# Kernel optimization log

Hardware: AMD Instinct MI355X
Metric: run time of the kernel (lower is better)

## Reference

```python
import jax, jax.numpy as jnp
import numpy as np

COST_KEYPOINT = 1.0
COST_GIOU = 1.0


def box_cxcyczwhd_to_xyzxyz(b):
    c, s = b[..., :3], b[..., 3:]
    return jnp.concatenate([c - 0.5 * s, c + 0.5 * s], axis=-1)


def generalized_3d_box_iou(b1, b2):
    # b1: [N,6], b2: [M,6], both xyzxyz. Returns [N,M] GIoU.
    vol1 = jnp.prod(b1[:, 3:] - b1[:, :3], axis=-1)
    vol2 = jnp.prod(b2[:, 3:] - b2[:, :3], axis=-1)
    lt = jnp.maximum(b1[:, None, :3], b2[None, :, :3])
    rb = jnp.minimum(b1[:, None, 3:], b2[None, :, 3:])
    inter = jnp.prod(jnp.maximum(rb - lt, 0.0), axis=-1)
    union = vol1[:, None] + vol2[None, :] - inter
    iou = inter / union
    elt = jnp.minimum(b1[:, None, :3], b2[None, :, :3])
    erb = jnp.maximum(b1[:, None, 3:], b2[None, :, 3:])
    evol = jnp.prod(jnp.maximum(erb - elt, 0.0), axis=-1)
    return iou - (evol - union) / evol


@jax.jit
def compute_cost(pred_keypoints, pred_boxes, tgt_boxes, tgt_keypoints):
    bs, Q = pred_keypoints.shape[:2]
    out_kp = pred_keypoints.reshape(bs * Q, -1)            # [bs*Q, K*3]
    out_boxes = pred_boxes.reshape(bs * Q, 6)
    tgt_b = tgt_boxes.reshape(-1, 6)                        # [T_total, 6]
    tgt_kp = tgt_keypoints.reshape(tgt_b.shape[0], -1)      # [T_total, K*3]
    xyz_min = box_cxcyczwhd_to_xyzxyz(tgt_b)[:, :3]
    K3 = tgt_kp.shape[-1]
    kp = tgt_kp.reshape(-1, K3 // 3, 3)
    # normalize keypoints relative to box min-corner and box size
    dist_kp = ((kp - xyz_min[:, None, :]) / tgt_b[:, None, 3:]).reshape(-1, K3)
    # L1 cdist: [bs*Q, T_total]
    cost_kp = jnp.sum(jnp.abs(out_kp[:, None, :] - dist_kp[None, :, :]), axis=-1)
    cost_giou = -generalized_3d_box_iou(
        box_cxcyczwhd_to_xyzxyz(out_boxes), box_cxcyczwhd_to_xyzxyz(tgt_b))
    C = COST_KEYPOINT * cost_kp + COST_GIOU * cost_giou
    return C.reshape(bs, Q, -1)


def _lap(cost):
    # Jonker-Volgenant shortest-augmenting-path LAP (scipy-style).
    # cost: [n, m] with n <= m. Returns (arange(n), col4row).
    cost = np.asarray(cost, dtype=np.float64)
    n, m = cost.shape
    u = np.zeros(n)
    v = np.zeros(m)
    col4row = np.full(n, -1, np.int64)
    row4col = np.full(m, -1, np.int64)
    for curRow in range(n):
        path = np.full(m, -1, np.int64)
        SR = np.zeros(n, bool)
        SC = np.zeros(m, bool)
        shortest = np.full(m, np.inf)
        minVal = 0.0
        i = curRow
        sink = -1
        while sink == -1:
            SR[i] = True
            idx = np.where(~SC)[0]
            r = minVal + cost[i, idx] - u[i] - v[idx]
            better = r < shortest[idx]
            shortest[idx[better]] = r[better]
            path[idx[better]] = i
            jloc = np.argmin(shortest[idx])
            j = idx[jloc]
            minVal = shortest[j]
            SC[j] = True
            if row4col[j] == -1:
                sink = j
            else:
                i = row4col[j]
        u[curRow] += minVal
        mask = SR.copy()
        mask[curRow] = False
        u[mask] += minVal - shortest[col4row[mask]]
        v[SC] -= minVal - shortest[SC]
        j = sink
        while True:
            i = path[j]
            row4col[j] = i
            col4row[i], j = j, col4row[i]
            if i == curRow:
                break
    return np.arange(n), col4row


def _linear_sum_assignment(cost):
    # cost: [Q, T] with Q >= T; mirrors scipy's transpose handling:
    # returns (row_ind sorted ascending, matching col_ind).
    rows, cols = _lap(cost.T)  # rows = arange(T) targets, cols = query ids
    order = np.argsort(cols)
    return cols[order], rows[order]


def setup_inputs() -> dict:
    key = jax.random.key(0)
    k1, k2, k3, k4, k5, k6 = jax.random.split(key, 6)
    BS, Q, T, K = 16, 300, 50, 17
    pred_keypoints = jax.random.normal(k1, (BS, Q, K * 3), dtype=jnp.float32)
    pred_boxes = jnp.concatenate([
        jax.random.uniform(k2, (BS, Q, 3), dtype=jnp.float32),
        jax.random.uniform(k3, (BS, Q, 3), dtype=jnp.float32) * 0.5 + 0.05,
    ], axis=-1)
    tgt_boxes = jnp.concatenate([
        jax.random.uniform(k4, (BS, T, 3), dtype=jnp.float32),
        jax.random.uniform(k5, (BS, T, 3), dtype=jnp.float32) * 0.5 + 0.05,
    ], axis=-1)
    tgt_keypoints = jax.random.uniform(k6, (BS, T, K * 3), dtype=jnp.float32)
    return {"pred_keypoints": pred_keypoints, "pred_boxes": pred_boxes,
            "tgt_boxes": tgt_boxes, "tgt_keypoints": tgt_keypoints}


def reference(pred_keypoints, pred_boxes, tgt_boxes, tgt_keypoints):
    C = compute_cost(pred_keypoints, pred_boxes, tgt_boxes, tgt_keypoints)
    Cn = np.asarray(C)
    bs, Q, _ = Cn.shape
    T = tgt_boxes.shape[1]
    # per-image block of the column-split cost matrix, as in torch C.split(sizes, -1)
    idx = []
    for b in range(bs):
        i, j = _linear_sum_assignment(Cn[b, :, b * T:(b + 1) * T])
        idx.append(np.stack([i, j]))
    indices = jnp.asarray(np.stack(idx), dtype=jnp.int32)  # [bs, 2, T]
    return C, indices
```

## Files before the change

### kernel.cpp

```cpp
#include <hip/hip_runtime.h>
#include <math.h>

#define BSZ 16
#define NQ 300
#define NT 50
#define K3 51
#define NPRED (BSZ*NQ)
#define NTGT  (BSZ*NT)
#define NC    (NPRED*NTGT)
#define TSTRIDE 301
#define SMEMF 15232


template<int CTRL, int RMASK>
__device__ __forceinline__ unsigned int dpp_minstep_u32(unsigned int x) {
    unsigned int o = (unsigned int)__builtin_amdgcn_update_dpp((int)x, (int)x, CTRL, RMASK, 0xF, false);
    return (x < o) ? x : o;
}
__device__ __forceinline__ unsigned int wave_min_u32(unsigned int x) {
    x = dpp_minstep_u32<0xB1, 0xF>(x);
    x = dpp_minstep_u32<0x4E, 0xF>(x);
    x = dpp_minstep_u32<0x141, 0xF>(x);
    x = dpp_minstep_u32<0x140, 0xF>(x);
    x = dpp_minstep_u32<0x142, 0xA>(x);
    x = dpp_minstep_u32<0x143, 0xC>(x);
    return (unsigned int)__builtin_amdgcn_readlane((int)x, 63);
}
__device__ __forceinline__ float readlane_f32(float x, int lane) {
    return __int_as_float(__builtin_amdgcn_readlane(__float_as_int(x), lane));
}
__device__ __forceinline__ unsigned int f32key(float x) {
    unsigned int b = (unsigned int)__float_as_int(x);
    return b ^ (((int)b < 0) ? 0xFFFFFFFFu : 0x80000000u);
}

__device__ __forceinline__ float giou_cost(
    float plt0, float plt1, float plt2, float prb0, float prb1, float prb2, float pvol,
    float tlt0, float tlt1, float tlt2, float trb0, float trb1, float trb2, float tvol)
{
    float inter = fmaxf(fminf(prb0,trb0) - fmaxf(plt0,tlt0), 0.f);
    inter *= fmaxf(fminf(prb1,trb1) - fmaxf(plt1,tlt1), 0.f);
    inter *= fmaxf(fminf(prb2,trb2) - fmaxf(plt2,tlt2), 0.f);
    float evol = fmaxf(fmaxf(prb0,trb0) - fminf(plt0,tlt0), 0.f);
    evol *= fmaxf(fmaxf(prb1,trb1) - fminf(plt1,tlt1), 0.f);
    evol *= fmaxf(fmaxf(prb2,trb2) - fminf(plt2,tlt2), 0.f);
    float uni = pvol + tvol - inter;
    return inter/uni - (evol - uni)/evol;
}

__global__ __launch_bounds__(1024) void fused_kernel(
    const float* __restrict__ pred_kp, const float* __restrict__ pred_boxes,
    const float* __restrict__ tgt_boxes, const float* __restrict__ tgt_kp,
    float* __restrict__ C, float* __restrict__ out_idx)
{
    __shared__ __align__(16) float smem[SMEMF];
    const int bid = blockIdx.x;
    const int tid = threadIdx.x;

    if (bid >= BSZ) {
        const int cb = bid - BSZ;
        const int pb = cb % 75, tb = cb / 75;
        const int p0 = pb * 64, t0 = tb * 80;
        float* s_dk   = smem;
        float* s_tbox = smem + 4480;
        float* s_pk   = smem + 5440;

        if (tid < 80) {
            const float* tb6 = tgt_boxes + (size_t)(t0 + tid) * 6;
            float c0=tb6[0], c1=tb6[1], c2=tb6[2], s0=tb6[3], s1=tb6[4], s2=tb6[5];
            float l0=c0-0.5f*s0, l1=c1-0.5f*s1, l2=c2-0.5f*s2;
            float r0=c0+0.5f*s0, r1=c1+0.5f*s1, r2=c2+0.5f*s2;
            float* tw = s_tbox + tid*12;
            tw[0]=l0; tw[1]=l1; tw[2]=l2; tw[3]=r0; tw[4]=r1; tw[5]=r2;
            tw[6]=(r0-l0)*(r1-l1)*(r2-l2);
            tw[9]=s0; tw[10]=s1; tw[11]=s2;
        }
        __syncthreads();
        for (int e = tid; e < 80*K3; e += 1024) {
            int t = e / K3; int c = e - t*K3; int d = c % 3;
            float kp = tgt_kp[(size_t)t0*K3 + e];
            s_dk[t*56 + c] = (kp - s_tbox[t*12 + d]) / s_tbox[t*12 + 9 + d];
        }
        for (int e = tid; e < 64*K3; e += 1024)
            s_pk[e] = pred_kp[(size_t)p0*K3 + e];
        __syncthreads();

        const int pl = tid & 63, g = tid >> 6;
        float a[K3];
        #pragma unroll
        for (int c = 0; c < K3; ++c) a[c] = s_pk[pl*K3 + c];
        const int p = p0 + pl;
        const float* pb6 = pred_boxes + (size_t)p * 6;
        float pc0=pb6[0],pc1=pb6[1],pc2=pb6[2],ps0=pb6[3],ps1=pb6[4],ps2=pb6[5];
        float plt0=pc0-0.5f*ps0, plt1=pc1-0.5f*ps1, plt2=pc2-0.5f*ps2;
        float prb0=pc0+0.5f*ps0, prb1=pc1+0.5f*ps1, prb2=pc2+0.5f*ps2;
        float pvol=(prb0-plt0)*(prb1-plt1)*(prb2-plt2);

        #pragma unroll
        for (int k = 0; k < 5; ++k) {
            int tl = g*5 + k;
            const float* bbp = s_dk + tl*56;
            float sum = 0.f;
            #pragma unroll
            for (int c4 = 0; c4 < 12; ++c4) {
                float4 q = *(const float4*)(bbp + 4*c4);
                sum += fabsf(a[4*c4+0] - q.x);
                sum += fabsf(a[4*c4+1] - q.y);
                sum += fabsf(a[4*c4+2] - q.z);
                sum += fabsf(a[4*c4+3] - q.w);
            }
            sum += fabsf(a[48] - bbp[48]);
            sum += fabsf(a[49] - bbp[49]);
            sum += fabsf(a[50] - bbp[50]);
            const float* tw = s_tbox + tl*12;
            float g_ = giou_cost(plt0,plt1,plt2,prb0,prb1,prb2,pvol,
                                 tw[0],tw[1],tw[2],tw[3],tw[4],tw[5],tw[6]);
            C[(size_t)p*NTGT + (t0+tl)] = sum - g_;
        }
        return;
    }

    const int b = bid;
    const int ln = tid & 63, w = tid >> 6;
    const int bq0 = b*NQ, bt0 = b*NT;
    float* tile = smem;

    for (int e = tid; e < NT*K3; e += 1024)
        tile[e] = tgt_kp[(size_t)bt0*K3 + e];
    __syncthreads();

    float dk[K3];
    float tl0=0,tl1=0,tl2=0,tr0=0,tr1=0,tr2=0,tvol=0;
    if (ln < NT) {
        const float* tb6 = tgt_boxes + (size_t)(bt0+ln)*6;
        float c0=tb6[0],c1=tb6[1],c2=tb6[2],s0=tb6[3],s1=tb6[4],s2=tb6[5];
        tl0=c0-0.5f*s0; tl1=c1-0.5f*s1; tl2=c2-0.5f*s2;
        tr0=c0+0.5f*s0; tr1=c1+0.5f*s1; tr2=c2+0.5f*s2;
        tvol=(tr0-tl0)*(tr1-tl1)*(tr2-tl2);
        #pragma unroll
        for (int c = 0; c < K3; ++c) {
            int d = c % 3;
            float L = (d==0)?tl0:((d==1)?tl1:tl2);
            float S = (d==0)?s0:((d==1)?s1:s2);
            dk[c] = (tile[ln*K3 + c] - L) / S;
        }
    }
    __syncthreads();

    for (int p = w; p < NQ; p += 16) {
        const float* prow = pred_kp + (size_t)(bq0+p)*K3;
        const float* pb6  = pred_boxes + (size_t)(bq0+p)*6;
        float pc0=pb6[0],pc1=pb6[1],pc2=pb6[2],ps0=pb6[3],ps1=pb6[4],ps2=pb6[5];
        float plt0=pc0-0.5f*ps0, plt1=pc1-0.5f*ps1, plt2=pc2-0.5f*ps2;
        float prb0=pc0+0.5f*ps0, prb1=pc1+0.5f*ps1, prb2=pc2+0.5f*ps2;
        float pvol=(prb0-plt0)*(prb1-plt1)*(prb2-plt2);
        if (ln < NT) {
            float sum = 0.f;
            #pragma unroll
            for (int c = 0; c < K3; ++c) sum += fabsf(prow[c] - dk[c]);
            float g_ = giou_cost(plt0,plt1,plt2,prb0,prb1,prb2,pvol,
                                 tl0,tl1,tl2,tr0,tr1,tr2,tvol);
            tile[ln*TSTRIDE + p] = sum - g_;
        }
    }
    __syncthreads();

    float* s_rmv = smem + 15072;
    int*   s_rmc = (int*)(smem + 15136);
    for (int r = w; r < NT; r += 16) {
        float bv = __builtin_inff(); int bj = 0x7fffffff;
        #pragma unroll
        for (int s = 0; s < 5; ++s) {
            int j = ln + 64*s;
            if (j < NQ) {
                float cv = tile[r*TSTRIDE + j];
                if (cv < bv || (cv == bv && j < bj)) { bv = cv; bj = j; }
            }
        }
        #pragma unroll
        for (int off = 32; off > 0; off >>= 1) {
            float ov = __shfl_xor(bv, off);
            int   oj = __shfl_xor(bj, off);
            if (ov < bv || (ov == bv && oj < bj)) { bv = ov; bj = oj; }
        }
        if (ln == 0) { s_rmv[r] = bv; s_rmc[r] = bj; }
    }
    __syncthreads();
    if (w != 0) return;

    float u = 0.0f;
    int c4r = -1;
    if (ln < NT) u = s_rmv[ln];
    int wantj = (ln < NT) ? s_rmc[ln] : -1;
    for (int r = 0; r < NT; ++r) {
        int j = __builtin_amdgcn_readlane(wantj, r);
        unsigned long long taken = __ballot((ln < NT) && (c4r == j));
        if (taken == 0ull && ln == r) c4r = j;
    }

    float v5[5], sh[5];
    int pth[5];
    #pragma unroll
    for (int s = 0; s < 5; ++s) v5[s] = 0.0f;
    const float FINF = __builtin_inff();

    for (int curRow = 0; curRow < NT; ++curRow) {
        if (__builtin_amdgcn_readlane(c4r, curRow) >= 0) continue;
        #pragma unroll
        for (int s = 0; s < 5; ++s) { sh[s] = FINF; pth[s] = -1; }
        int SCm = (ln < 60) ? 0 : 0x1F;
        unsigned long long SRmask = 0ull;
        int i = curRow;
        float minVal = 0.0f;
        int sink = -1;

        while (true) {
            SRmask |= (1ull << i);
            float cf[5] = {0.f, 0.f, 0.f, 0.f, 0.f};
            if (ln < 60) {
                const float* rp = tile + i*TSTRIDE + 5*ln;
                cf[0]=rp[0]; cf[1]=rp[1]; cf[2]=rp[2]; cf[3]=rp[3]; cf[4]=rp[4];
            }
            float u_i = readlane_f32(u, i);
            float e[5];
            #pragma unroll
            for (int s = 0; s < 5; ++s) {
                bool open = ((SCm >> s) & 1) == 0;
                float r = ((minVal + cf[s]) - u_i) - v5[s];
                bool upd = open && (r < sh[s]);
                sh[s]  = upd ? r : sh[s];
                pth[s] = upd ? i : pth[s];
                e[s] = open ? sh[s] : FINF;
            }
            float lmin = fminf(fminf(fminf(e[0], e[1]), fminf(e[2], e[3])), e[4]);
            int aslot = (e[0]==lmin) ? 0 : (e[1]==lmin) ? 1 :
                        (e[2]==lmin) ? 2 : (e[3]==lmin) ? 3 : 4;
            unsigned int kmin = wave_min_u32(f32key(lmin));
            unsigned long long cands = __ballot(f32key(lmin) == kmin);
            int lstar = __builtin_ctzll(cands);
            float m = readlane_f32(lmin, lstar);
            int jstar = 5*lstar + __builtin_amdgcn_readlane(aslot, lstar);
            minVal = m;
            unsigned long long mm = __ballot((ln < NT) && (c4r == jstar));
            if (ln == lstar) SCm |= 1 << (jstar - 5*lstar);
            if (mm == 0ull) { sink = jstar; break; }
            i = __builtin_ctzll(mm);
        }

        int cg  = (c4r >= 0) ? c4r : 0;
        int gow = cg / 5, gsl = cg - 5*gow;
        float g0 = __shfl(sh[0], gow);
        float g1 = __shfl(sh[1], gow);
        float g2 = __shfl(sh[2], gow);
        float g3 = __shfl(sh[3], gow);
        float g4 = __shfl(sh[4], gow);
        float gg = g0;
        gg = (gsl == 1) ? g1 : gg;
        gg = (gsl == 2) ? g2 : gg;
        gg = (gsl == 3) ? g3 : gg;
        gg = (gsl == 4) ? g4 : gg;
        bool inSR = (ln < NT) && ((SRmask >> ln) & 1ull);
        float du = (ln == curRow) ? minVal : (minVal - gg);
        u = inSR ? (u + du) : u;
        #pragma unroll
        for (int s = 0; s < 5; ++s) {
            bool closed = ((SCm >> s) & 1) != 0;
            v5[s] = closed ? (v5[s] - (minVal - sh[s])) : v5[s];
        }

        int j = sink;
        while (true) {
            int ow2 = j / 5, sl2 = j - 5*ow2;
            int ps = pth[0];
            ps = (sl2==1) ? pth[1] : ps;
            ps = (sl2==2) ? pth[2] : ps;
            ps = (sl2==3) ? pth[3] : ps;
            ps = (sl2==4) ? pth[4] : ps;
            int ii = __builtin_amdgcn_readlane(ps, ow2);
            int jj = __builtin_amdgcn_readlane(c4r, ii);
            if (ln == ii) c4r = j;
            j = jj;
            if (ii == curRow) break;
        }
    }

    int* smem_i = (int*)smem;
    __threadfence_block();
    if (ln < NT) smem_i[ln] = c4r;
    __threadfence_block();
    int myc = c4r;
    int rank = 0;
    for (int s2 = 0; s2 < NT; ++s2) rank += (smem_i[s2] < myc) ? 1 : 0;
    if (ln < NT) {
        out_idx[b*(2*NT) + rank]      = (float)myc;
        out_idx[b*(2*NT) + NT + rank] = (float)ln;
    }
}

extern "C" void kernel_launch(void* const* d_in, const int* in_sizes, int n_in,
                              void* d_out, int out_size, void* d_ws, size_t ws_size,
                              hipStream_t stream)
{
    const float* pred_kp    = (const float*)d_in[0];
    const float* pred_boxes = (const float*)d_in[1];
    const float* tgt_boxes  = (const float*)d_in[2];
    const float* tgt_kp     = (const float*)d_in[3];
    float* C   = (float*)d_out;
    float* idx = C + NC;
    fused_kernel<<<dim3(BSZ + 750), 1024, 0, stream>>>(
        pred_kp, pred_boxes, tgt_boxes, tgt_kp, C, idx);
}
```

Before: 127.9 us.

## Split fused kernel into cost and LAP kernels with register-resident cost rows

Splits the single fused launch into a cost-matrix kernel and a separate LAP kernel. The LAP kernel now runs with 256 threads and reads its per-image block back from the global C instead of recomputing it. It also preloads each lane's 5 columns for all 50 rows into registers and picks the row with a switch, instead of reading shared memory on every augmenting step. The goal is to free the cost kernel from the LAP's heavy shared-memory and register footprint and to shorten the serial LAP inner loop, at the cost of an extra launch and a dependency on global memory.

```diff
diff --git a/kernel.cpp b/kernel.cpp
--- a/kernel.cpp
+++ b/kernel.cpp
@@ -9,7 +9,6 @@
 #define NTGT  (BSZ*NT)
 #define NC    (NPRED*NTGT)
 #define TSTRIDE 301
-#define SMEMF 15232
 
 
 template<int CTRL, int RMASK>
@@ -48,126 +47,96 @@
     return inter/uni - (evol - uni)/evol;
 }
 
-__global__ __launch_bounds__(1024) void fused_kernel(
+__global__ __launch_bounds__(1024) void cost_kernel(
     const float* __restrict__ pred_kp, const float* __restrict__ pred_boxes,
     const float* __restrict__ tgt_boxes, const float* __restrict__ tgt_kp,
-    float* __restrict__ C, float* __restrict__ out_idx)
+    float* __restrict__ C)
 {
-    __shared__ __align__(16) float smem[SMEMF];
-    const int bid = blockIdx.x;
+    __shared__ __align__(16) float smem[8704];
+    const int cb = blockIdx.x;
     const int tid = threadIdx.x;
-
-    if (bid >= BSZ) {
-        const int cb = bid - BSZ;
-        const int pb = cb % 75, tb = cb / 75;
-        const int p0 = pb * 64, t0 = tb * 80;
-        float* s_dk   = smem;
-        float* s_tbox = smem + 4480;
-        float* s_pk   = smem + 5440;
-
-        if (tid < 80) {
-            const float* tb6 = tgt_boxes + (size_t)(t0 + tid) * 6;
-            float c0=tb6[0], c1=tb6[1], c2=tb6[2], s0=tb6[3], s1=tb6[4], s2=tb6[5];
-            float l0=c0-0.5f*s0, l1=c1-0.5f*s1, l2=c2-0.5f*s2;
-            float r0=c0+0.5f*s0, r1=c1+0.5f*s1, r2=c2+0.5f*s2;
-            float* tw = s_tbox + tid*12;
-            tw[0]=l0; tw[1]=l1; tw[2]=l2; tw[3]=r0; tw[4]=r1; tw[5]=r2;
-            tw[6]=(r0-l0)*(r1-l1)*(r2-l2);
-            tw[9]=s0; tw[10]=s1; tw[11]=s2;
-        }
-        __syncthreads();
-        for (int e = tid; e < 80*K3; e += 1024) {
-            int t = e / K3; int c = e - t*K3; int d = c % 3;
-            float kp = tgt_kp[(size_t)t0*K3 + e];
-            s_dk[t*56 + c] = (kp - s_tbox[t*12 + d]) / s_tbox[t*12 + 9 + d];
-        }
-        for (int e = tid; e < 64*K3; e += 1024)
-            s_pk[e] = pred_kp[(size_t)p0*K3 + e];
-        __syncthreads();
-
-        const int pl = tid & 63, g = tid >> 6;
-        float a[K3];
-        #pragma unroll
-        for (int c = 0; c < K3; ++c) a[c] = s_pk[pl*K3 + c];
-        const int p = p0 + pl;
-        const float* pb6 = pred_boxes + (size_t)p * 6;
-        float pc0=pb6[0],pc1=pb6[1],pc2=pb6[2],ps0=pb6[3],ps1=pb6[4],ps2=pb6[5];
-        float plt0=pc0-0.5f*ps0, plt1=pc1-0.5f*ps1, plt2=pc2-0.5f*ps2;
-        float prb0=pc0+0.5f*ps0, prb1=pc1+0.5f*ps1, prb2=pc2+0.5f*ps2;
-        float pvol=(prb0-plt0)*(prb1-plt1)*(prb2-plt2);
-
-        #pragma unroll
-        for (int k = 0; k < 5; ++k) {
-            int tl = g*5 + k;
-            const float* bbp = s_dk + tl*56;
-            float sum = 0.f;
-            #pragma unroll
-            for (int c4 = 0; c4 < 12; ++c4) {
-                float4 q = *(const float4*)(bbp + 4*c4);
-                sum += fabsf(a[4*c4+0] - q.x);
-                sum += fabsf(a[4*c4+1] - q.y);
-                sum += fabsf(a[4*c4+2] - q.z);
-                sum += fabsf(a[4*c4+3] - q.w);
-            }
-            sum += fabsf(a[48] - bbp[48]);
-            sum += fabsf(a[49] - bbp[49]);
-            sum += fabsf(a[50] - bbp[50]);
-            const float* tw = s_tbox + tl*12;
-            float g_ = giou_cost(plt0,plt1,plt2,prb0,prb1,prb2,pvol,
-                                 tw[0],tw[1],tw[2],tw[3],tw[4],tw[5],tw[6]);
-            C[(size_t)p*NTGT + (t0+tl)] = sum - g_;
-        }
-        return;
-    }
-
-    const int b = bid;
+    const int pb = cb % 75, tb = cb / 75;
+    const int p0 = pb * 64, t0 = tb * 80;
+    float* s_dk   = smem;
+    float* s_tbox = smem + 4480;
+    float* s_pk   = smem + 5440;
+
+    if (tid < 80) {
+        const float* tb6 = tgt_boxes + (size_t)(t0 + tid) * 6;
+        float c0=tb6[0], c1=tb6[1], c2=tb6[2], s0=tb6[3], s1=tb6[4], s2=tb6[5];
+        float l0=c0-0.5f*s0, l1=c1-0.5f*s1, l2=c2-0.5f*s2;
+        float r0=c0+0.5f*s0, r1=c1+0.5f*s1, r2=c2+0.5f*s2;
+        float* tw = s_tbox + tid*12;
+        tw[0]=l0; tw[1]=l1; tw[2]=l2; tw[3]=r0; tw[4]=r1; tw[5]=r2;
+        tw[6]=(r0-l0)*(r1-l1)*(r2-l2);
+        tw[9]=s0; tw[10]=s1; tw[11]=s2;
+    }
+    __syncthreads();
+    for (int e = tid; e < 80*K3; e += 1024) {
+        int t = e / K3; int c = e - t*K3; int d = c % 3;
+        float kp = tgt_kp[(size_t)t0*K3 + e];
+        s_dk[t*56 + c] = (kp - s_tbox[t*12 + d]) / s_tbox[t*12 + 9 + d];
+    }
+    for (int e = tid; e < 64*K3; e += 1024)
+        s_pk[e] = pred_kp[(size_t)p0*K3 + e];
+    __syncthreads();
+
+    const int pl = tid & 63, g = tid >> 6;
+    float a[K3];
+    #pragma unroll
+    for (int c = 0; c < K3; ++c) a[c] = s_pk[pl*K3 + c];
+    const int p = p0 + pl;
+    const float* pb6 = pred_boxes + (size_t)p * 6;
+    float pc0=pb6[0],pc1=pb6[1],pc2=pb6[2],ps0=pb6[3],ps1=pb6[4],ps2=pb6[5];
+    float plt0=pc0-0.5f*ps0, plt1=pc1-0.5f*ps1, plt2=pc2-0.5f*ps2;
+    float prb0=pc0+0.5f*ps0, prb1=pc1+0.5f*ps1, prb2=pc2+0.5f*ps2;
+    float pvol=(prb0-plt0)*(prb1-plt1)*(prb2-plt2);
+
+    #pragma unroll
+    for (int k = 0; k < 5; ++k) {
+        int tl = g*5 + k;
+        const float* bbp = s_dk + tl*56;
+        float sum = 0.f;
+        #pragma unroll
+        for (int c4 = 0; c4 < 12; ++c4) {
+            float4 q = *(const float4*)(bbp + 4*c4);
+            sum += fabsf(a[4*c4+0] - q.x);
+            sum += fabsf(a[4*c4+1] - q.y);
+            sum += fabsf(a[4*c4+2] - q.z);
+            sum += fabsf(a[4*c4+3] - q.w);
+        }
+        sum += fabsf(a[48] - bbp[48]);
+        sum += fabsf(a[49] - bbp[49]);
+        sum += fabsf(a[50] - bbp[50]);
+        const float* tw = s_tbox + tl*12;
+        float g_ = giou_cost(plt0,plt1,plt2,prb0,prb1,prb2,pvol,
+                             tw[0],tw[1],tw[2],tw[3],tw[4],tw[5],tw[6]);
+        C[(size_t)p*NTGT + (t0+tl)] = sum - g_;
+    }
+}
+
+#define RCASE(I) case I: cf[0]=rt[5*I+0]; cf[1]=rt[5*I+1]; cf[2]=rt[5*I+2]; \
+                          cf[3]=rt[5*I+3]; cf[4]=rt[5*I+4]; break;
+
+__global__ __launch_bounds__(256, 1) void lap_kernel(
+    const float* __restrict__ C, float* __restrict__ out_idx)
+{
+    __shared__ __align__(16) float smem[15232];
+    const int b = blockIdx.x;
+    const int tid = threadIdx.x;
     const int ln = tid & 63, w = tid >> 6;
     const int bq0 = b*NQ, bt0 = b*NT;
     float* tile = smem;
 
-    for (int e = tid; e < NT*K3; e += 1024)
-        tile[e] = tgt_kp[(size_t)bt0*K3 + e];
-    __syncthreads();
-
-    float dk[K3];
-    float tl0=0,tl1=0,tl2=0,tr0=0,tr1=0,tr2=0,tvol=0;
-    if (ln < NT) {
-        const float* tb6 = tgt_boxes + (size_t)(bt0+ln)*6;
-        float c0=tb6[0],c1=tb6[1],c2=tb6[2],s0=tb6[3],s1=tb6[4],s2=tb6[5];
-        tl0=c0-0.5f*s0; tl1=c1-0.5f*s1; tl2=c2-0.5f*s2;
-        tr0=c0+0.5f*s0; tr1=c1+0.5f*s1; tr2=c2+0.5f*s2;
-        tvol=(tr0-tl0)*(tr1-tl1)*(tr2-tl2);
-        #pragma unroll
-        for (int c = 0; c < K3; ++c) {
-            int d = c % 3;
-            float L = (d==0)?tl0:((d==1)?tl1:tl2);
-            float S = (d==0)?s0:((d==1)?s1:s2);
-            dk[c] = (tile[ln*K3 + c] - L) / S;
-        }
-    }
-    __syncthreads();
-
-    for (int p = w; p < NQ; p += 16) {
-        const float* prow = pred_kp + (size_t)(bq0+p)*K3;
-        const float* pb6  = pred_boxes + (size_t)(bq0+p)*6;
-        float pc0=pb6[0],pc1=pb6[1],pc2=pb6[2],ps0=pb6[3],ps1=pb6[4],ps2=pb6[5];
-        float plt0=pc0-0.5f*ps0, plt1=pc1-0.5f*ps1, plt2=pc2-0.5f*ps2;
-        float prb0=pc0+0.5f*ps0, prb1=pc1+0.5f*ps1, prb2=pc2+0.5f*ps2;
-        float pvol=(prb0-plt0)*(prb1-plt1)*(prb2-plt2);
-        if (ln < NT) {
-            float sum = 0.f;
-            #pragma unroll
-            for (int c = 0; c < K3; ++c) sum += fabsf(prow[c] - dk[c]);
-            float g_ = giou_cost(plt0,plt1,plt2,prb0,prb1,prb2,pvol,
-                                 tl0,tl1,tl2,tr0,tr1,tr2,tvol);
-            tile[ln*TSTRIDE + p] = sum - g_;
-        }
+    for (int e = tid; e < NQ*NT; e += 256) {
+        int p = e / NT, t = e - p*NT;
+        tile[t*TSTRIDE + p] = C[(size_t)(bq0+p)*NTGT + bt0 + t];
     }
     __syncthreads();
 
     float* s_rmv = smem + 15072;
     int*   s_rmc = (int*)(smem + 15136);
-    for (int r = w; r < NT; r += 16) {
+    for (int r = w; r < NT; r += 4) {
         float bv = __builtin_inff(); int bj = 0x7fffffff;
         #pragma unroll
         for (int s = 0; s < 5; ++s) {
@@ -187,6 +156,17 @@
     }
     __syncthreads();
     if (w != 0) return;
+
+    float rt[NT*5];
+    {
+        const float* base = tile + 5*ln;
+        #pragma unroll
+        for (int i2 = 0; i2 < NT; ++i2) {
+            #pragma unroll
+            for (int s = 0; s < 5; ++s)
+                rt[i2*5+s] = base[i2*TSTRIDE + s];
+        }
+    }
 
     float u = 0.0f;
     int c4r = -1;
@@ -216,10 +196,20 @@
 
         while (true) {
             SRmask |= (1ull << i);
-            float cf[5] = {0.f, 0.f, 0.f, 0.f, 0.f};
-            if (ln < 60) {
-                const float* rp = tile + i*TSTRIDE + 5*ln;
-                cf[0]=rp[0]; cf[1]=rp[1]; cf[2]=rp[2]; cf[3]=rp[3]; cf[4]=rp[4];
+            float cf[5];
+            switch (i) {
+                RCASE(0)  RCASE(1)  RCASE(2)  RCASE(3)  RCASE(4)
+                RCASE(5)  RCASE(6)  RCASE(7)  RCASE(8)  RCASE(9)
+                RCASE(10) RCASE(11) RCASE(12) RCASE(13) RCASE(14)
+                RCASE(15) RCASE(16) RCASE(17) RCASE(18) RCASE(19)
+                RCASE(20) RCASE(21) RCASE(22) RCASE(23) RCASE(24)
+                RCASE(25) RCASE(26) RCASE(27) RCASE(28) RCASE(29)
+                RCASE(30) RCASE(31) RCASE(32) RCASE(33) RCASE(34)
+                RCASE(35) RCASE(36) RCASE(37) RCASE(38) RCASE(39)
+                RCASE(40) RCASE(41) RCASE(42) RCASE(43) RCASE(44)
+                RCASE(45) RCASE(46) RCASE(47) RCASE(48)
+                default:  cf[0]=rt[245]; cf[1]=rt[246]; cf[2]=rt[247];
+                          cf[3]=rt[248]; cf[4]=rt[249]; break;
             }
             float u_i = readlane_f32(u, i);
             float e[5];
@@ -307,6 +297,6 @@
     const float* tgt_kp     = (const float*)d_in[3];
     float* C   = (float*)d_out;
     float* idx = C + NC;
-    fused_kernel<<<dim3(BSZ + 750), 1024, 0, stream>>>(
-        pred_kp, pred_boxes, tgt_boxes, tgt_kp, C, idx);
-}
+    cost_kernel<<<dim3(750), 1024, 0, stream>>>(pred_kp, pred_boxes, tgt_boxes, tgt_kp, C);
+    lap_kernel<<<dim3(BSZ), 256, 0, stream>>>(C, idx);
+}
```

After: 134.3 us. +4.9%, slower.

## Cache LAP cost rows in registers and shrink blocks to 256 threads

Applied to the files above, without the earlier changes.

Before the serial LAP loop, each lane of the solver wave copies its five-column slice of all 50 cost rows from LDS into a 250-entry register array. The inner loop then picks the current row through a 50-way switch, taking the LDS load off the critical path of the augmenting-path search. The block size drops from 1024 to 256 threads with launch_bounds(256,1), so each thread does more cost-matrix work and the compiler gets a large register budget. The infinite loops become bounded guard loops, and lanes 60–63 now read slice values past the 300 valid columns instead of zeros, which could affect correctness if those slots are not masked.

```diff
diff --git a/kernel.cpp b/kernel.cpp
--- a/kernel.cpp
+++ b/kernel.cpp
@@ -48,7 +48,10 @@
     return inter/uni - (evol - uni)/evol;
 }
 
-__global__ __launch_bounds__(1024) void fused_kernel(
+#define RCASE(I) case I: cf[0]=rt[5*I+0]; cf[1]=rt[5*I+1]; cf[2]=rt[5*I+2]; \
+                          cf[3]=rt[5*I+3]; cf[4]=rt[5*I+4]; break;
+
+__global__ __launch_bounds__(256, 1) void fused_kernel(
     const float* __restrict__ pred_kp, const float* __restrict__ pred_boxes,
     const float* __restrict__ tgt_boxes, const float* __restrict__ tgt_kp,
     float* __restrict__ C, float* __restrict__ out_idx)
@@ -76,12 +79,12 @@
             tw[9]=s0; tw[10]=s1; tw[11]=s2;
         }
         __syncthreads();
-        for (int e = tid; e < 80*K3; e += 1024) {
+        for (int e = tid; e < 80*K3; e += 256) {
             int t = e / K3; int c = e - t*K3; int d = c % 3;
             float kp = tgt_kp[(size_t)t0*K3 + e];
             s_dk[t*56 + c] = (kp - s_tbox[t*12 + d]) / s_tbox[t*12 + 9 + d];
         }
-        for (int e = tid; e < 64*K3; e += 1024)
+        for (int e = tid; e < 64*K3; e += 256)
             s_pk[e] = pred_kp[(size_t)p0*K3 + e];
         __syncthreads();
 
@@ -97,8 +100,8 @@
         float pvol=(prb0-plt0)*(prb1-plt1)*(prb2-plt2);
 
         #pragma unroll
-        for (int k = 0; k < 5; ++k) {
-            int tl = g*5 + k;
+        for (int k = 0; k < 20; ++k) {
+            int tl = g*20 + k;
             const float* bbp = s_dk + tl*56;
             float sum = 0.f;
             #pragma unroll
@@ -125,7 +128,7 @@
     const int bq0 = b*NQ, bt0 = b*NT;
     float* tile = smem;
 
-    for (int e = tid; e < NT*K3; e += 1024)
+    for (int e = tid; e < NT*K3; e += 256)
         tile[e] = tgt_kp[(size_t)bt0*K3 + e];
     __syncthreads();
 
@@ -147,7 +150,7 @@
     }
     __syncthreads();
 
-    for (int p = w; p < NQ; p += 16) {
+    for (int p = w; p < NQ; p += 4) {
         const float* prow = pred_kp + (size_t)(bq0+p)*K3;
         const float* pb6  = pred_boxes + (size_t)(bq0+p)*6;
         float pc0=pb6[0],pc1=pb6[1],pc2=pb6[2],ps0=pb6[3],ps1=pb6[4],ps2=pb6[5];
@@ -167,7 +170,7 @@
 
     float* s_rmv = smem + 15072;
     int*   s_rmc = (int*)(smem + 15136);
-    for (int r = w; r < NT; r += 16) {
+    for (int r = w; r < NT; r += 4) {
         float bv = __builtin_inff(); int bj = 0x7fffffff;
         #pragma unroll
         for (int s = 0; s < 5; ++s) {
@@ -187,6 +190,17 @@
     }
     __syncthreads();
     if (w != 0) return;
+
+    float rt[NT*5];
+    {
+        const float* base = tile + 5*ln;
+        #pragma unroll
+        for (int i2 = 0; i2 < NT; ++i2) {
+            #pragma unroll
+            for (int s = 0; s < 5; ++s)
+                rt[i2*5+s] = base[i2*TSTRIDE + s];
+        }
+    }
 
     float u = 0.0f;
     int c4r = -1;
@@ -214,12 +228,22 @@
         float minVal = 0.0f;
         int sink = -1;
 
-        while (true) {
+        for (int guard = 0; guard < 512; ++guard) {
             SRmask |= (1ull << i);
-            float cf[5] = {0.f, 0.f, 0.f, 0.f, 0.f};
-            if (ln < 60) {
-                const float* rp = tile + i*TSTRIDE + 5*ln;
-                cf[0]=rp[0]; cf[1]=rp[1]; cf[2]=rp[2]; cf[3]=rp[3]; cf[4]=rp[4];
+            float cf[5];
+            switch (i) {
+                RCASE(0)  RCASE(1)  RCASE(2)  RCASE(3)  RCASE(4)
+                RCASE(5)  RCASE(6)  RCASE(7)  RCASE(8)  RCASE(9)
+                RCASE(10) RCASE(11) RCASE(12) RCASE(13) RCASE(14)
+                RCASE(15) RCASE(16) RCASE(17) RCASE(18) RCASE(19)
+                RCASE(20) RCASE(21) RCASE(22) RCASE(23) RCASE(24)
+                RCASE(25) RCASE(26) RCASE(27) RCASE(28) RCASE(29)
+                RCASE(30) RCASE(31) RCASE(32) RCASE(33) RCASE(34)
+                RCASE(35) RCASE(36) RCASE(37) RCASE(38) RCASE(39)
+                RCASE(40) RCASE(41) RCASE(42) RCASE(43) RCASE(44)
+                RCASE(45) RCASE(46) RCASE(47) RCASE(48)
+                default:  cf[0]=rt[245]; cf[1]=rt[246]; cf[2]=rt[247];
+                          cf[3]=rt[248]; cf[4]=rt[249]; break;
             }
             float u_i = readlane_f32(u, i);
             float e[5];
@@ -246,6 +270,7 @@
             if (mm == 0ull) { sink = jstar; break; }
             i = __builtin_ctzll(mm);
         }
+        if (sink < 0) continue;
 
         int cg  = (c4r >= 0) ? c4r : 0;
         int gow = cg / 5, gsl = cg - 5*gow;
@@ -269,7 +294,7 @@
         }
 
         int j = sink;
-        while (true) {
+        for (int guard = 0; guard < 64; ++guard) {
             int ow2 = j / 5, sl2 = j - 5*ow2;
             int ps = pth[0];
             ps = (sl2==1) ? pth[1] : ps;
@@ -307,6 +332,6 @@
     const float* tgt_kp     = (const float*)d_in[3];
     float* C   = (float*)d_out;
     float* idx = C + NC;
-    fused_kernel<<<dim3(BSZ + 750), 1024, 0, stream>>>(
+    fused_kernel<<<dim3(BSZ + 750), 256, 0, stream>>>(
         pred_kp, pred_boxes, tgt_boxes, tgt_kp, C, idx);
 }
```

Result: slower. 147.1 us (+15.0%).

## Interleave two LAP solves per wave to hide serial latency

Applied to the files above, without the earlier changes.

Each LAP block now handles two images. It builds both cost tiles in shared memory, then runs the two Jonker-Volgenant shortest-path searches interleaved in one wavefront, stepping both in lockstep. The goal is to overlap the long dependent chains of readlane, ballot and DPP reductions of two independent problems, so serial latency is hidden by instruction-level parallelism. The cost is doubled shared memory and registers, more serial cost-tile setup per block, and half as many LAP blocks.

```diff
diff --git a/kernel.cpp b/kernel.cpp
--- a/kernel.cpp
+++ b/kernel.cpp
@@ -9,7 +9,9 @@
 #define NTGT  (BSZ*NT)
 #define NC    (NPRED*NTGT)
 #define TSTRIDE 301
-#define SMEMF 15232
+#define TILEF 15232
+#define SMEMF (2*TILEF)
+#define NLAP 8
 
 
 template<int CTRL, int RMASK>
@@ -57,8 +59,8 @@
     const int bid = blockIdx.x;
     const int tid = threadIdx.x;
 
-    if (bid >= BSZ) {
-        const int cb = bid - BSZ;
+    if (bid >= NLAP) {
+        const int cb = bid - NLAP;
         const int pb = cb % 75, tb = cb / 75;
         const int p0 = pb * 64, t0 = tb * 80;
         float* s_dk   = smem;
@@ -120,117 +122,154 @@
         return;
     }
 
-    const int b = bid;
     const int ln = tid & 63, w = tid >> 6;
-    const int bq0 = b*NQ, bt0 = b*NT;
-    float* tile = smem;
-
-    for (int e = tid; e < NT*K3; e += 1024)
-        tile[e] = tgt_kp[(size_t)bt0*K3 + e];
-    __syncthreads();
-
-    float dk[K3];
-    float tl0=0,tl1=0,tl2=0,tr0=0,tr1=0,tr2=0,tvol=0;
-    if (ln < NT) {
-        const float* tb6 = tgt_boxes + (size_t)(bt0+ln)*6;
-        float c0=tb6[0],c1=tb6[1],c2=tb6[2],s0=tb6[3],s1=tb6[4],s2=tb6[5];
-        tl0=c0-0.5f*s0; tl1=c1-0.5f*s1; tl2=c2-0.5f*s2;
-        tr0=c0+0.5f*s0; tr1=c1+0.5f*s1; tr2=c2+0.5f*s2;
-        tvol=(tr0-tl0)*(tr1-tl1)*(tr2-tl2);
-        #pragma unroll
-        for (int c = 0; c < K3; ++c) {
-            int d = c % 3;
-            float L = (d==0)?tl0:((d==1)?tl1:tl2);
-            float S = (d==0)?s0:((d==1)?s1:s2);
-            dk[c] = (tile[ln*K3 + c] - L) / S;
-        }
+
+    for (int side = 0; side < 2; ++side) {
+        const int bb = 2*bid + side;
+        const int bq0 = bb*NQ, bt0 = bb*NT;
+        float* tile  = smem + side*TILEF;
+        float* s_rmv = tile + 15072;
+        int*   s_rmc = (int*)(tile + 15136);
+
+        for (int e = tid; e < NT*K3; e += 1024)
+            tile[e] = tgt_kp[(size_t)bt0*K3 + e];
+        __syncthreads();
+
+        float dk[K3];
+        float tl0=0,tl1=0,tl2=0,tr0=0,tr1=0,tr2=0,tvol=0;
+        if (ln < NT) {
+            const float* tb6 = tgt_boxes + (size_t)(bt0+ln)*6;
+            float c0=tb6[0],c1=tb6[1],c2=tb6[2],s0=tb6[3],s1=tb6[4],s2=tb6[5];
+            tl0=c0-0.5f*s0; tl1=c1-0.5f*s1; tl2=c2-0.5f*s2;
+            tr0=c0+0.5f*s0; tr1=c1+0.5f*s1; tr2=c2+0.5f*s2;
+            tvol=(tr0-tl0)*(tr1-tl1)*(tr2-tl2);
+            #pragma unroll
+            for (int c = 0; c < K3; ++c) {
+                int d = c % 3;
+                float L = (d==0)?tl0:((d==1)?tl1:tl2);
+                float S = (d==0)?s0:((d==1)?s1:s2);
+                dk[c] = (tile[ln*K3 + c] - L) / S;
+            }
+        }
+        __syncthreads();
+
+        for (int p = w; p < NQ; p += 16) {
+            const float* prow = pred_kp + (size_t)(bq0+p)*K3;
+            const float* pb6  = pred_boxes + (size_t)(bq0+p)*6;
+            float pc0=pb6[0],pc1=pb6[1],pc2=pb6[2],ps0=pb6[3],ps1=pb6[4],ps2=pb6[5];
+            float plt0=pc0-0.5f*ps0, plt1=pc1-0.5f*ps1, plt2=pc2-0.5f*ps2;
+            float prb0=pc0+0.5f*ps0, prb1=pc1+0.5f*ps1, prb2=pc2+0.5f*ps2;
+            float pvol=(prb0-plt0)*(prb1-plt1)*(prb2-plt2);
+            if (ln < NT) {
+                float sum = 0.f;
+                #pragma unroll
+                for (int c = 0; c < K3; ++c) sum += fabsf(prow[c] - dk[c]);
+                float g_ = giou_cost(plt0,plt1,plt2,prb0,prb1,prb2,pvol,
+                                     tl0,tl1,tl2,tr0,tr1,tr2,tvol);
+                tile[ln*TSTRIDE + p] = sum - g_;
+            }
+        }
+        __syncthreads();
+
+        for (int r = w; r < NT; r += 16) {
+            float bv = __builtin_inff(); int bj = 0x7fffffff;
+            #pragma unroll
+            for (int s = 0; s < 5; ++s) {
+                int j = ln + 64*s;
+                if (j < NQ) {
+                    float cv = tile[r*TSTRIDE + j];
+                    if (cv < bv || (cv == bv && j < bj)) { bv = cv; bj = j; }
+                }
+            }
+            #pragma unroll
+            for (int off = 32; off > 0; off >>= 1) {
+                float ov = __shfl_xor(bv, off);
+                int   oj = __shfl_xor(bj, off);
+                if (ov < bv || (ov == bv && oj < bj)) { bv = ov; bj = oj; }
+            }
+            if (ln == 0) { s_rmv[r] = bv; s_rmc[r] = bj; }
+        }
+        __syncthreads();
     }
-    __syncthreads();
-
-    for (int p = w; p < NQ; p += 16) {
-        const float* prow = pred_kp + (size_t)(bq0+p)*K3;
-        const float* pb6  = pred_boxes + (size_t)(bq0+p)*6;
-        float pc0=pb6[0],pc1=pb6[1],pc2=pb6[2],ps0=pb6[3],ps1=pb6[4],ps2=pb6[5];
-        float plt0=pc0-0.5f*ps0, plt1=pc1-0.5f*ps1, plt2=pc2-0.5f*ps2;
-        float prb0=pc0+0.5f*ps0, prb1=pc1+0.5f*ps1, prb2=pc2+0.5f*ps2;
-        float pvol=(prb0-plt0)*(prb1-plt1)*(prb2-plt2);
-        if (ln < NT) {
-            float sum = 0.f;
-            #pragma unroll
-            for (int c = 0; c < K3; ++c) sum += fabsf(prow[c] - dk[c]);
-            float g_ = giou_cost(plt0,plt1,plt2,prb0,prb1,prb2,pvol,
-                                 tl0,tl1,tl2,tr0,tr1,tr2,tvol);
-            tile[ln*TSTRIDE + p] = sum - g_;
-        }
-    }
-    __syncthreads();
-
-    float* s_rmv = smem + 15072;
-    int*   s_rmc = (int*)(smem + 15136);
-    for (int r = w; r < NT; r += 16) {
-        float bv = __builtin_inff(); int bj = 0x7fffffff;
-        #pragma unroll
-        for (int s = 0; s < 5; ++s) {
-            int j = ln + 64*s;
-            if (j < NQ) {
-                float cv = tile[r*TSTRIDE + j];
-                if (cv < bv || (cv == bv && j < bj)) { bv = cv; bj = j; }
-            }
-        }
-        #pragma unroll
-        for (int off = 32; off > 0; off >>= 1) {
-            float ov = __shfl_xor(bv, off);
-            int   oj = __shfl_xor(bj, off);
-            if (ov < bv || (ov == bv && oj < bj)) { bv = ov; bj = oj; }
-        }
-        if (ln == 0) { s_rmv[r] = bv; s_rmc[r] = bj; }
-    }
-    __syncthreads();
     if (w != 0) return;
 
-    float u = 0.0f;
-    int c4r = -1;
-    if (ln < NT) u = s_rmv[ln];
-    int wantj = (ln < NT) ? s_rmc[ln] : -1;
-    for (int r = 0; r < NT; ++r) {
-        int j = __builtin_amdgcn_readlane(wantj, r);
-        unsigned long long taken = __ballot((ln < NT) && (c4r == j));
-        if (taken == 0ull && ln == r) c4r = j;
-    }
-
-    float v5[5], sh[5];
-    int pth[5];
+    float* tileA = smem;          float* tileB = smem + TILEF;
+    float* rmvA  = tileA + 15072; float* rmvB  = tileB + 15072;
+    int*   rmcA  = (int*)(tileA + 15136); int* rmcB = (int*)(tileB + 15136);
+    const float FINF = __builtin_inff();
+
+    float uA = 0.f; int c4rA = -1;
+    if (ln < NT) uA = rmvA[ln];
+    { int wantj = (ln < NT) ? rmcA[ln] : -1;
+      for (int r = 0; r < NT; ++r) {
+          int j = __builtin_amdgcn_readlane(wantj, r);
+          unsigned long long tk = __ballot((ln < NT) && (c4rA == j));
+          if (tk == 0ull && ln == r) c4rA = j;
+      } }
+    float uB = 0.f; int c4rB = -1;
+    if (ln < NT) uB = rmvB[ln];
+    { int wantj = (ln < NT) ? rmcB[ln] : -1;
+      for (int r = 0; r < NT; ++r) {
+          int j = __builtin_amdgcn_readlane(wantj, r);
+          unsigned long long tk = __ballot((ln < NT) && (c4rB == j));
+          if (tk == 0ull && ln == r) c4rB = j;
+      } }
+
+    float vA[5], vB[5], shA[5], shB[5];
+    int pthA[5], pthB[5];
     #pragma unroll
-    for (int s = 0; s < 5; ++s) v5[s] = 0.0f;
-    const float FINF = __builtin_inff();
-
-    for (int curRow = 0; curRow < NT; ++curRow) {
-        if (__builtin_amdgcn_readlane(c4r, curRow) >= 0) continue;
-        #pragma unroll
-        for (int s = 0; s < 5; ++s) { sh[s] = FINF; pth[s] = -1; }
-        int SCm = (ln < 60) ? 0 : 0x1F;
-        unsigned long long SRmask = 0ull;
-        int i = curRow;
-        float minVal = 0.0f;
-        int sink = -1;
-
-        while (true) {
-            SRmask |= (1ull << i);
-            float cf[5] = {0.f, 0.f, 0.f, 0.f, 0.f};
-            if (ln < 60) {
-                const float* rp = tile + i*TSTRIDE + 5*ln;
-                cf[0]=rp[0]; cf[1]=rp[1]; cf[2]=rp[2]; cf[3]=rp[3]; cf[4]=rp[4];
-            }
-            float u_i = readlane_f32(u, i);
+    for (int s = 0; s < 5; ++s) { vA[s] = 0.f; vB[s] = 0.f; }
+
+    int crA = 0, crB = 0, iA = 0, iB = 0, sinkA = -1, sinkB = -1;
+    int SCmA = 0, SCmB = 0;
+    unsigned long long SRA = 0ull, SRB = 0ull;
+    float mvA = 0.f, mvB = 0.f;
+    bool actA = false, actB = false, doneA = false, doneB = false;
+
+    for (int tick = 0; tick < 4096; ++tick) {
+        if (!actA && !doneA) {
+            while (crA < NT && __builtin_amdgcn_readlane(c4rA, crA) >= 0) ++crA;
+            if (crA >= NT) doneA = true;
+            else {
+                #pragma unroll
+                for (int s = 0; s < 5; ++s) { shA[s] = FINF; pthA[s] = -1; }
+                SCmA = (ln < 60) ? 0 : 0x1F; SRA = 0ull; iA = crA; mvA = 0.f; sinkA = -1; actA = true;
+            }
+        }
+        if (!actB && !doneB) {
+            while (crB < NT && __builtin_amdgcn_readlane(c4rB, crB) >= 0) ++crB;
+            if (crB >= NT) doneB = true;
+            else {
+                #pragma unroll
+                for (int s = 0; s < 5; ++s) { shB[s] = FINF; pthB[s] = -1; }
+                SCmB = (ln < 60) ? 0 : 0x1F; SRB = 0ull; iB = crB; mvB = 0.f; sinkB = -1; actB = true;
+            }
+        }
+        if (doneA && doneB) break;
+
+        float cfA[5] = {0,0,0,0,0}, cfB[5] = {0,0,0,0,0};
+        if (actA && ln < 60) {
+            const float* rp = tileA + iA*TSTRIDE + 5*ln;
+            cfA[0]=rp[0]; cfA[1]=rp[1]; cfA[2]=rp[2]; cfA[3]=rp[3]; cfA[4]=rp[4];
+        }
+        if (actB && ln < 60) {
+            const float* rp = tileB + iB*TSTRIDE + 5*ln;
+            cfB[0]=rp[0]; cfB[1]=rp[1]; cfB[2]=rp[2]; cfB[3]=rp[3]; cfB[4]=rp[4];
+        }
+
+        bool finA = false, finB = false;
+        if (actA) {
+            SRA |= 1ull << iA;
+            float u_i = readlane_f32(uA, iA);
             float e[5];
             #pragma unroll
             for (int s = 0; s < 5; ++s) {
-                bool open = ((SCm >> s) & 1) == 0;
-                float r = ((minVal + cf[s]) - u_i) - v5[s];
-                bool upd = open && (r < sh[s]);
-                sh[s]  = upd ? r : sh[s];
-                pth[s] = upd ? i : pth[s];
-                e[s] = open ? sh[s] : FINF;
+                bool open = ((SCmA >> s) & 1) == 0;
+                float r = ((mvA + cfA[s]) - u_i) - vA[s];
+                bool upd = open && (r < shA[s]);
+                shA[s]  = upd ? r : shA[s];
+                pthA[s] = upd ? iA : pthA[s];
+                e[s] = open ? shA[s] : FINF;
             }
             float lmin = fminf(fminf(fminf(e[0], e[1]), fminf(e[2], e[3])), e[4]);
             int aslot = (e[0]==lmin) ? 0 : (e[1]==lmin) ? 1 :
@@ -240,60 +279,127 @@
             int lstar = __builtin_ctzll(cands);
             float m = readlane_f32(lmin, lstar);
             int jstar = 5*lstar + __builtin_amdgcn_readlane(aslot, lstar);
-            minVal = m;
-            unsigned long long mm = __ballot((ln < NT) && (c4r == jstar));
-            if (ln == lstar) SCm |= 1 << (jstar - 5*lstar);
-            if (mm == 0ull) { sink = jstar; break; }
-            i = __builtin_ctzll(mm);
-        }
-
-        int cg  = (c4r >= 0) ? c4r : 0;
-        int gow = cg / 5, gsl = cg - 5*gow;
-        float g0 = __shfl(sh[0], gow);
-        float g1 = __shfl(sh[1], gow);
-        float g2 = __shfl(sh[2], gow);
-        float g3 = __shfl(sh[3], gow);
-        float g4 = __shfl(sh[4], gow);
-        float gg = g0;
-        gg = (gsl == 1) ? g1 : gg;
-        gg = (gsl == 2) ? g2 : gg;
-        gg = (gsl == 3) ? g3 : gg;
-        gg = (gsl == 4) ? g4 : gg;
-        bool inSR = (ln < NT) && ((SRmask >> ln) & 1ull);
-        float du = (ln == curRow) ? minVal : (minVal - gg);
-        u = inSR ? (u + du) : u;
-        #pragma unroll
-        for (int s = 0; s < 5; ++s) {
-            bool closed = ((SCm >> s) & 1) != 0;
-            v5[s] = closed ? (v5[s] - (minVal - sh[s])) : v5[s];
-        }
-
-        int j = sink;
-        while (true) {
-            int ow2 = j / 5, sl2 = j - 5*ow2;
-            int ps = pth[0];
-            ps = (sl2==1) ? pth[1] : ps;
-            ps = (sl2==2) ? pth[2] : ps;
-            ps = (sl2==3) ? pth[3] : ps;
-            ps = (sl2==4) ? pth[4] : ps;
-            int ii = __builtin_amdgcn_readlane(ps, ow2);
-            int jj = __builtin_amdgcn_readlane(c4r, ii);
-            if (ln == ii) c4r = j;
-            j = jj;
-            if (ii == curRow) break;
+            mvA = m;
+            unsigned long long mm = __ballot((ln < NT) && (c4rA == jstar));
+            if (ln == lstar) SCmA |= 1 << (jstar - 5*lstar);
+            if (mm == 0ull) { sinkA = jstar; actA = false; finA = true; }
+            else iA = __builtin_ctzll(mm);
+        }
+        if (actB) {
+            SRB |= 1ull << iB;
+            float u_i = readlane_f32(uB, iB);
+            float e[5];
+            #pragma unroll
+            for (int s = 0; s < 5; ++s) {
+                bool open = ((SCmB >> s) & 1) == 0;
+                float r = ((mvB + cfB[s]) - u_i) - vB[s];
+                bool upd = open && (r < shB[s]);
+                shB[s]  = upd ? r : shB[s];
+                pthB[s] = upd ? iB : pthB[s];
+                e[s] = open ? shB[s] : FINF;
+            }
+            float lmin = fminf(fminf(fminf(e[0], e[1]), fminf(e[2], e[3])), e[4]);
+            int aslot = (e[0]==lmin) ? 0 : (e[1]==lmin) ? 1 :
+                        (e[2]==lmin) ? 2 : (e[3]==lmin) ? 3 : 4;
+            unsigned int kmin = wave_min_u32(f32key(lmin));
+            unsigned long long cands = __ballot(f32key(lmin) == kmin);
+            int lstar = __builtin_ctzll(cands);
+            float m = readlane_f32(lmin, lstar);
+            int jstar = 5*lstar + __builtin_amdgcn_readlane(aslot, lstar);
+            mvB = m;
+            unsigned long long mm = __ballot((ln < NT) && (c4rB == jstar));
+            if (ln == lstar) SCmB |= 1 << (jstar - 5*lstar);
+            if (mm == 0ull) { sinkB = jstar; actB = false; finB = true; }
+            else iB = __builtin_ctzll(mm);
+        }
+
+        if (finA) {
+            int cg  = (c4rA >= 0) ? c4rA : 0;
+            int gow = cg / 5, gsl = cg - 5*gow;
+            float g0 = __shfl(shA[0], gow), g1 = __shfl(shA[1], gow);
+            float g2 = __shfl(shA[2], gow), g3 = __shfl(shA[3], gow);
+            float g4 = __shfl(shA[4], gow);
+            float gg = g0;
+            gg = (gsl == 1) ? g1 : gg; gg = (gsl == 2) ? g2 : gg;
+            gg = (gsl == 3) ? g3 : gg; gg = (gsl == 4) ? g4 : gg;
+            bool inSR = (ln < NT) && ((SRA >> ln) & 1ull);
+            float du = (ln == crA) ? mvA : (mvA - gg);
+            uA = inSR ? (uA + du) : uA;
+            #pragma unroll
+            for (int s = 0; s < 5; ++s) {
+                bool closed = ((SCmA >> s) & 1) != 0;
+                vA[s] = closed ? (vA[s] - (mvA - shA[s])) : vA[s];
+            }
+            int j = sinkA;
+            for (int g2_ = 0; g2_ < 64; ++g2_) {
+                int ow2 = j / 5, sl2 = j - 5*ow2;
+                int ps = pthA[0];
+                ps = (sl2==1) ? pthA[1] : ps; ps = (sl2==2) ? pthA[2] : ps;
+                ps = (sl2==3) ? pthA[3] : ps; ps = (sl2==4) ? pthA[4] : ps;
+                int ii = __builtin_amdgcn_readlane(ps, ow2);
+                int jj = __builtin_amdgcn_readlane(c4rA, ii);
+                if (ln == ii) c4rA = j;
+                j = jj;
+                if (ii == crA) break;
+            }
+        }
+        if (finB) {
+            int cg  = (c4rB >= 0) ? c4rB : 0;
+            int gow = cg / 5, gsl = cg - 5*gow;
+            float g0 = __shfl(shB[0], gow), g1 = __shfl(shB[1], gow);
+            float g2 = __shfl(shB[2], gow), g3 = __shfl(shB[3], gow);
+            float g4 = __shfl(shB[4], gow);
+            float gg = g0;
+            gg = (gsl == 1) ? g1 : gg; gg = (gsl == 2) ? g2 : gg;
+            gg = (gsl == 3) ? g3 : gg; gg = (gsl == 4) ? g4 : gg;
+            bool inSR = (ln < NT) && ((SRB >> ln) & 1ull);
+            float du = (ln == crB) ? mvB : (mvB - gg);
+            uB = inSR ? (uB + du) : uB;
+            #pragma unroll
+            for (int s = 0; s < 5; ++s) {
+                bool closed = ((SCmB >> s) & 1) != 0;
+                vB[s] = closed ? (vB[s] - (mvB - shB[s])) : vB[s];
+            }
+            int j = sinkB;
+            for (int g2_ = 0; g2_ < 64; ++g2_) {
+                int ow2 = j / 5, sl2 = j - 5*ow2;
+                int ps = pthB[0];
+                ps = (sl2==1) ? pthB[1] : ps; ps = (sl2==2) ? pthB[2] : ps;
+                ps = (sl2==3) ? pthB[3] : ps; ps = (sl2==4) ? pthB[4] : ps;
+                int ii = __builtin_amdgcn_readlane(ps, ow2);
+                int jj = __builtin_amdgcn_readlane(c4rB, ii);
+                if (ln == ii) c4rB = j;
+                j = jj;
+                if (ii == crB) break;
+            }
         }
     }
 
-    int* smem_i = (int*)smem;
-    __threadfence_block();
-    if (ln < NT) smem_i[ln] = c4r;
-    __threadfence_block();
-    int myc = c4r;
-    int rank = 0;
-    for (int s2 = 0; s2 < NT; ++s2) rank += (smem_i[s2] < myc) ? 1 : 0;
-    if (ln < NT) {
-        out_idx[b*(2*NT) + rank]      = (float)myc;
-        out_idx[b*(2*NT) + NT + rank] = (float)ln;
+    {
+        int* smem_i = (int*)tileA;
+        __threadfence_block();
+        if (ln < NT) smem_i[ln] = c4rA;
+        __threadfence_block();
+        int myc = c4rA, rank = 0;
+        for (int s2 = 0; s2 < NT; ++s2) rank += (smem_i[s2] < myc) ? 1 : 0;
+        const int bA = 2*bid;
+        if (ln < NT) {
+            out_idx[bA*(2*NT) + rank]      = (float)myc;
+            out_idx[bA*(2*NT) + NT + rank] = (float)ln;
+        }
+    }
+    {
+        int* smem_i = (int*)tileB;
+        __threadfence_block();
+        if (ln < NT) smem_i[ln] = c4rB;
+        __threadfence_block();
+        int myc = c4rB, rank = 0;
+        for (int s2 = 0; s2 < NT; ++s2) rank += (smem_i[s2] < myc) ? 1 : 0;
+        const int bB = 2*bid + 1;
+        if (ln < NT) {
+            out_idx[bB*(2*NT) + rank]      = (float)myc;
+            out_idx[bB*(2*NT) + NT + rank] = (float)ln;
+        }
     }
 }
 
@@ -307,6 +413,6 @@
     const float* tgt_kp     = (const float*)d_in[3];
     float* C   = (float*)d_out;
     float* idx = C + NC;
-    fused_kernel<<<dim3(BSZ + 750), 1024, 0, stream>>>(
+    fused_kernel<<<dim3(NLAP + 750), 1024, 0, stream>>>(
         pred_kp, pred_boxes, tgt_boxes, tgt_kp, C, idx);
 }
```

Measured after the change: 198.4 us. 1.55x slower.
